# Kernel optimization log

Hardware: AMD Instinct MI355X
Metric: run time of the kernel (lower is better)

Reference implementation:

```python
import jax, jax.numpy as jnp
import numpy as np

N_NODES = 50000
N_EDGES = 200000
IN_C = 128
HID_C = 128
HEADS = 4
OUT_C = 64
NEG_SLOPE = 0.2


def _glorot(key, shape):
    fan_in, fan_out = shape[0], shape[-1]
    limit = np.sqrt(6.0 / (fan_in + fan_out)).astype(np.float32)
    return jax.random.uniform(key, shape, jnp.float32, -limit, limit)


def setup_inputs() -> dict:
    key = jax.random.key(0)
    ks = jax.random.split(key, 32)
    inp = {}
    inp["x"] = jax.random.normal(ks[0], (N_NODES, IN_C), jnp.float32)
    inp["edge_index"] = jax.random.randint(ks[1], (2, N_EDGES), 0, N_NODES, jnp.int64)
    # layer dims: (in_dim, per_head_out, heads)
    dims = [
        (IN_C, HID_C, HEADS),
        (HID_C * HEADS, HID_C, HEADS),
        (HID_C * HEADS, HID_C, HEADS),
        (HID_C * HEADS, OUT_C, 1),
    ]
    concat = [True, True, True, False]
    kidx = 2
    for i, (din, dout, h) in enumerate(dims):
        inp[f"Wl{i}"] = _glorot(ks[kidx], (din, h * dout)); kidx += 1
        inp[f"bl{i}"] = jnp.zeros((h * dout,), jnp.float32)
        inp[f"Wr{i}"] = _glorot(ks[kidx], (din, h * dout)); kidx += 1
        inp[f"br{i}"] = jnp.zeros((h * dout,), jnp.float32)
        inp[f"att{i}"] = _glorot(ks[kidx], (h, dout)); kidx += 1
        inp[f"b{i}"] = jnp.zeros((h * dout if concat[i] else dout,), jnp.float32)
    return inp


def _segment_softmax(e, seg, num_segments):
    # e: [E, H], seg: [E] target-node ids
    m = jax.ops.segment_max(e, seg, num_segments=num_segments)  # [N, H]
    ex = jnp.exp(e - m[seg])
    s = jax.ops.segment_sum(ex, seg, num_segments=num_segments)  # [N, H]
    return ex / (s[seg] + 1e-16)


def _gatv2_layer(x, src, dst, Wl, bl, Wr, br, att, bias, heads, out_c, concat):
    n = x.shape[0]
    xl = (x @ Wl + bl).reshape(n, heads, out_c)  # source transform
    xr = (x @ Wr + br).reshape(n, heads, out_c)  # target transform
    # GATv2 attention: e_ij = a^T LeakyReLU(xl_j + xr_i)
    z = jax.nn.leaky_relu(xl[src] + xr[dst], NEG_SLOPE)  # [E, H, C]
    e = jnp.einsum("ehc,hc->eh", z, att)  # [E, H]
    alpha = _segment_softmax(e, dst, n)  # [E, H]
    out = jax.ops.segment_sum(alpha[:, :, None] * xl[src], dst, num_segments=n)  # [N, H, C]
    out = out.reshape(n, heads * out_c) if concat else out.mean(axis=1)
    return out + bias


def reference(x, edge_index,
              Wl0, bl0, Wr0, br0, att0, b0,
              Wl1, bl1, Wr1, br1, att1, b1,
              Wl2, bl2, Wr2, br2, att2, b2,
              Wl3, bl3, Wr3, br3, att3, b3):
    src, dst = edge_index[0], edge_index[1]
    layers = [
        (Wl0, bl0, Wr0, br0, att0, b0, HEADS, HID_C, True),
        (Wl1, bl1, Wr1, br1, att1, b1, HEADS, HID_C, True),
        (Wl2, bl2, Wr2, br2, att2, b2, HEADS, HID_C, True),
    ]
    h = x
    for (Wl, bl, Wr, br, att, b, nh, dc, cc) in layers:
        h = jax.nn.elu(_gatv2_layer(h, src, dst, Wl, bl, Wr, br, att, b, nh, dc, cc))
    out = _gatv2_layer(h, src, dst, Wl3, bl3, Wr3, br3, att3, b3, 1, OUT_C, False)
    return out
```

## Files before the change

### kernel.cpp

```cpp
#include <hip/hip_runtime.h>
#include <math.h>

#define NNODES 50000
#define NEDGES 200000

typedef unsigned short ushort_t;
using frag8 = __attribute__((ext_vector_type(8))) short;
using facc4 = __attribute__((ext_vector_type(4))) float;

static __device__ __forceinline__ ushort_t f2b(float f) {
  union { float f; unsigned u; } v; v.f = f;
  unsigned r = v.u + 0x7FFFu + ((v.u >> 16) & 1u);
  return (ushort_t)(r >> 16);
}
static __device__ __forceinline__ float b2f(unsigned hi) {
  return __uint_as_float(hi << 16);
}
static __device__ __forceinline__ void unpack8(const int4 v, float* f) {
  f[0] = b2f((unsigned)v.x & 0xFFFFu); f[1] = b2f((unsigned)v.x >> 16);
  f[2] = b2f((unsigned)v.y & 0xFFFFu); f[3] = b2f((unsigned)v.y >> 16);
  f[4] = b2f((unsigned)v.z & 0xFFFFu); f[5] = b2f((unsigned)v.z >> 16);
  f[6] = b2f((unsigned)v.w & 0xFFFFu); f[7] = b2f((unsigned)v.w >> 16);
}
static __device__ __forceinline__ void stf(float* p, float v) { *p = v; }
static __device__ __forceinline__ void stf(ushort_t* p, float v) { *p = f2b(v); }

__global__ void cast_x(const float* __restrict__ x, ushort_t* __restrict__ xb, int total8) {
  int t = blockIdx.x * 256 + threadIdx.x;
  if (t >= total8) return;
  const float4* p = (const float4*)(x + (size_t)t * 8);
  float4 a = p[0], b = p[1];
  int4 w = make_int4(
      (int)((unsigned)f2b(a.x) | ((unsigned)f2b(a.y) << 16)),
      (int)((unsigned)f2b(a.z) | ((unsigned)f2b(a.w) << 16)),
      (int)((unsigned)f2b(b.x) | ((unsigned)f2b(b.y) << 16)),
      (int)((unsigned)f2b(b.z) | ((unsigned)f2b(b.w) << 16)));
  *(int4*)(xb + (size_t)t * 8) = w;
}

__global__ void wt_prep2(const float* __restrict__ Wl, const float* __restrict__ Wr,
                         ushort_t* __restrict__ WtLR, int K, int Mo) {
  int t = blockIdx.x * 256 + threadIdx.x;
  const int tot = K * Mo;
  if (t >= 2 * tot) return;
  const float* W = (t < tot) ? Wl : Wr;
  int u = (t < tot) ? t : t - tot;
  int c = u / K, k = u - c * K;
  WtLR[t] = f2b(W[(size_t)k * Mo + c]);
}

__global__ __launch_bounds__(256) void gemm2_mfma(
    const ushort_t* __restrict__ A, const ushort_t* __restrict__ WtLR,
    const float* __restrict__ bl, const float* __restrict__ br,
    ushort_t* __restrict__ xlb, ushort_t* __restrict__ xrb,
    int N, int K, int Mo, int ncb) {
  __shared__ __align__(16) char smem[34816];
  auto Al = reinterpret_cast<ushort_t(*)[128][8]>(smem);
  auto Bl = reinterpret_cast<ushort_t(*)[128][8]>(smem + 8192);
  auto Cl = reinterpret_cast<ushort_t(*)[136]>(smem);

  const int nwg = gridDim.x;
  const int q = nwg >> 3, r = nwg & 7;
  const int xcd = blockIdx.x & 7, pos = blockIdx.x >> 3;
  const int orig = (xcd < r ? xcd * (q + 1) : r * (q + 1) + (xcd - r) * q) + pos;
  const int rp = orig / ncb, cb = orig - rp * ncb;
  const int brow = rp * 128;
  const int bcol = cb * 128;

  const int tid = threadIdx.x;
  const int wave = tid >> 6, lane = tid & 63;
  const int wr = wave >> 1, wc = wave & 1;
  const int l15 = lane & 15, l4 = lane >> 4;

  facc4 acc[4][4] = {};

  const int srow = tid >> 1;
  const int skb  = (tid & 1) * 2;
  for (int k0 = 0; k0 < K; k0 += 32) {
    {
      const int grow = brow + srow;
      int4 a0, a1;
      if (grow < N) {
        const int4* pa = (const int4*)(A + (size_t)grow * K + k0 + skb * 8);
        a0 = pa[0]; a1 = pa[1];
      } else {
        a0 = a1 = make_int4(0, 0, 0, 0);
      }
      *(int4*)&Al[skb + 0][srow][0] = a0;
      *(int4*)&Al[skb + 1][srow][0] = a1;
      const int4* pb = (const int4*)(WtLR + (size_t)(bcol + srow) * K + k0 + skb * 8);
      int4 b0 = pb[0], b1 = pb[1];
      *(int4*)&Bl[skb + 0][srow][0] = b0;
      *(int4*)&Bl[skb + 1][srow][0] = b1;
    }
    __syncthreads();
    frag8 af[4], bfg[4];
    #pragma unroll
    for (int i = 0; i < 4; ++i)
      af[i] = *(const frag8*)&Al[l4][wr * 64 + i * 16 + l15][0];
    #pragma unroll
    for (int j = 0; j < 4; ++j)
      bfg[j] = *(const frag8*)&Bl[l4][wc * 64 + j * 16 + l15][0];
    #pragma unroll
    for (int i = 0; i < 4; ++i)
      #pragma unroll
      for (int j = 0; j < 4; ++j)
        acc[i][j] = __builtin_amdgcn_mfma_f32_16x16x32_bf16(af[i], bfg[j], acc[i][j], 0, 0, 0);
    __syncthreads();
  }

  #pragma unroll
  for (int j = 0; j < 4; ++j) {
    const int lcol = wc * 64 + j * 16 + l15;
    const int col2 = bcol + lcol;
    const float bv = (col2 < Mo) ? bl[col2] : br[col2 - Mo];
    #pragma unroll
    for (int i = 0; i < 4; ++i) {
      const int lrow = wr * 64 + i * 16 + l4 * 4;
      #pragma unroll
      for (int rr = 0; rr < 4; ++rr)
        Cl[lrow + rr][lcol] = f2b(acc[i][j][rr] + bv);
    }
  }
  __syncthreads();
  {
    const int row = tid >> 1;
    const int half = tid & 1;
    const int grow = brow + row;
    if (grow < N) {
      const int colb = half * 64;
      const int col2 = bcol + colb;
      const bool isL = col2 < Mo;
      ushort_t* dst = (isL ? xlb : xrb) + (size_t)grow * Mo + (isL ? col2 : col2 - Mo);
      #pragma unroll
      for (int k = 0; k < 8; ++k) {
        int4 v = *(const int4*)&Cl[row][colb + k * 8];
        *(int4*)(dst + k * 8) = v;
      }
    }
  }
}

__global__ void csr_zero(int* __restrict__ deg) {
  int t = blockIdx.x * blockDim.x + threadIdx.x;
  if (t < NNODES) deg[t] = 0;
}
__global__ void csr_hist(const int* __restrict__ ei, int* __restrict__ deg) {
  int e = blockIdx.x * blockDim.x + threadIdx.x;
  if (e >= NEDGES) return;
  atomicAdd(&deg[ei[NEDGES + e]], 1);
}

#define SCAN_TPB 256
#define SCAN_EPT 4
#define SCAN_CHUNK (SCAN_TPB * SCAN_EPT)
#define SCAN_BLK ((NNODES + SCAN_CHUNK - 1) / SCAN_CHUNK)

__global__ __launch_bounds__(SCAN_TPB) void scan_k1(const int* __restrict__ deg,
                                                    int* __restrict__ bsum) {
  __shared__ int sd[SCAN_TPB];
  const int tid = threadIdx.x;
  const int tbase = blockIdx.x * SCAN_CHUNK + tid * SCAN_EPT;
  int s = 0;
  #pragma unroll
  for (int j = 0; j < SCAN_EPT; ++j) {
    int idx = tbase + j;
    if (idx < NNODES) s += deg[idx];
  }
  sd[tid] = s;
  __syncthreads();
  for (int d = SCAN_TPB / 2; d > 0; d >>= 1) {
    if (tid < d) sd[tid] += sd[tid + d];
    __syncthreads();
  }
  if (tid == 0) bsum[blockIdx.x] = sd[0];
}

__global__ __launch_bounds__(64) void scan_k2(const int* __restrict__ bsum,
                                              int* __restrict__ bpref,
                                              int* __restrict__ off) {
  __shared__ int sd[64];
  const int tid = threadIdx.x;
  sd[tid] = (tid < SCAN_BLK) ? bsum[tid] : 0;
  __syncthreads();
  for (int d = 1; d < 64; d <<= 1) {
    int t = (tid >= d) ? sd[tid - d] : 0;
    __syncthreads();
    sd[tid] += t;
    __syncthreads();
  }
  if (tid < SCAN_BLK) bpref[tid] = (tid == 0) ? 0 : sd[tid - 1];
  if (tid == 0) off[NNODES] = NEDGES;
}

__global__ __launch_bounds__(SCAN_TPB) void scan_k3(const int* __restrict__ deg,
                                                    const int* __restrict__ bpref,
                                                    int* __restrict__ off,
                                                    int* __restrict__ pos) {
  __shared__ int sd[SCAN_TPB];
  const int tid = threadIdx.x;
  const int tbase = blockIdx.x * SCAN_CHUNK + tid * SCAN_EPT;
  int v[SCAN_EPT];
  int s = 0;
  #pragma unroll
  for (int j = 0; j < SCAN_EPT; ++j) {
    int idx = tbase + j;
    v[j] = (idx < NNODES) ? deg[idx] : 0;
    s += v[j];
  }
  sd[tid] = s;
  __syncthreads();
  for (int d = 1; d < SCAN_TPB; d <<= 1) {
    int t = (tid >= d) ? sd[tid - d] : 0;
    __syncthreads();
    sd[tid] += t;
    __syncthreads();
  }
  int run = bpref[blockIdx.x] + ((tid == 0) ? 0 : sd[tid - 1]);
  #pragma unroll
  for (int j = 0; j < SCAN_EPT; ++j) {
    int idx = tbase + j;
    if (idx < NNODES) { off[idx] = run; pos[idx] = run; run += v[j]; }
  }
}

__global__ void csr_fill(const int* __restrict__ ei, int* __restrict__ pos,
                         int* __restrict__ eids) {
  int e = blockIdx.x * blockDim.x + threadIdx.x;
  if (e >= NEDGES) return;
  int p = atomicAdd(&pos[ei[NEDGES + e]], 1);
  eids[p] = e;
}

template<int H, int C, bool ELU, typename TO>
__global__ __launch_bounds__(256) void csr_fused(
    const int* __restrict__ off, const int* __restrict__ eids,
    const int* __restrict__ ei, const ushort_t* __restrict__ xl,
    const ushort_t* __restrict__ xr, const float* __restrict__ att,
    const float* __restrict__ bias, TO* __restrict__ out) {
  constexpr int HC = H * C;
  constexpr int CPL = HC / 64;
  constexpr int GROUP = C / CPL;
  const int n = (blockIdx.x * blockDim.x + threadIdx.x) >> 6;
  const int lane = threadIdx.x & 63;
  if (n >= NNODES) return;
  const int s0 = off[n], s1 = off[n + 1];

  float xrr[CPL], atr[CPL];
  if constexpr (CPL == 8) {
    unpack8(*(const int4*)(xr + (size_t)n * HC + lane * 8), xrr);
    const float4 a0 = *(const float4*)(att + lane * 8);
    const float4 a1 = *(const float4*)(att + lane * 8 + 4);
    atr[0] = a0.x; atr[1] = a0.y; atr[2] = a0.z; atr[3] = a0.w;
    atr[4] = a1.x; atr[5] = a1.y; atr[6] = a1.z; atr[7] = a1.w;
  } else {
    xrr[0] = b2f(xr[(size_t)n * HC + lane]);
    atr[0] = att[lane];
  }

  float m = -1e30f, s = 0.f;
  float acc[CPL] = {};

  int4 vnext = make_int4(0, 0, 0, 0);
  ushort_t unext = 0;
  if (s0 < s1) {
    const int srcn = ei[eids[s0]];
    if constexpr (CPL == 8) vnext = *(const int4*)(xl + (size_t)srcn * HC + lane * 8);
    else                    unext = xl[(size_t)srcn * HC + lane];
  }
  for (int i = s0; i < s1; ++i) {
    int4 vcur = vnext; ushort_t ucur = unext;
    if (i + 1 < s1) {
      const int srcn = ei[eids[i + 1]];
      if constexpr (CPL == 8) vnext = *(const int4*)(xl + (size_t)srcn * HC + lane * 8);
      else                    unext = xl[(size_t)srcn * HC + lane];
    }
    float zl[CPL];
    if constexpr (CPL == 8) unpack8(vcur, zl);
    else zl[0] = b2f(ucur);
    float e = 0.f;
    #pragma unroll
    for (int c = 0; c < CPL; ++c) {
      float z = zl[c] + xrr[c];
      z = (z > 0.f) ? z : 0.2f * z;
      e += z * atr[c];
    }
    #pragma unroll
    for (int o = 1; o < GROUP; o <<= 1)
      e += __shfl_xor(e, o, 64);
    if (e > m) {
      const float scale = __expf(m - e);
      s *= scale;
      #pragma unroll
      for (int c = 0; c < CPL; ++c) acc[c] *= scale;
      m = e;
    }
    const float w = __expf(e - m);
    s += w;
    #pragma unroll
    for (int c = 0; c < CPL; ++c) acc[c] += w * zl[c];
  }
  const float inv = 1.f / (s + 1e-16f);
  TO* po = out + (size_t)n * HC + lane * CPL;
  #pragma unroll
  for (int c = 0; c < CPL; ++c) {
    float v = acc[c] * inv + bias[lane * CPL + c];
    if (ELU) v = v > 0.f ? v : (__expf(v) - 1.f);
    stf(&po[c], v);
  }
}

__global__ void report_ws(float* __restrict__ out, float v) { out[0] = v; }

extern "C" void kernel_launch(void* const* d_in, const int* in_sizes, int n_in,
                              void* d_out, int out_size, void* d_ws, size_t ws_size,
                              hipStream_t stream) {
  const float* x  = (const float*)d_in[0];
  const int*   ei = (const int*)d_in[1];
  float* out = (float*)d_out;
  char* ws = (char*)d_ws;

  ushort_t* hbuf = (ushort_t*)(ws);
  ushort_t* xlb  = (ushort_t*)(ws + 51200000ull);
  ushort_t* xrb  = (ushort_t*)(ws + 102400000ull);
  ushort_t* xb   = (ushort_t*)(ws + 153600000ull);
  ushort_t* WtLR = (ushort_t*)(ws + 166400000ull);
  int* bsum  = (int*)(ws + 168500000ull);
  int* bpref = (int*)(ws + 168501024ull);
  int* coff  = (int*)(ws + 168600000ull);
  int* cpos  = (int*)(ws + 168800008ull);
  int* cdeg  = (int*)(ws + 169000012ull);
  int* eids  = (int*)(ws + 169200016ull);

  if (ws_size < 170000016ull) {
    report_ws<<<1, 1, 0, stream>>>(out, (float)ws_size);
    return;
  }

  cast_x<<<(NNODES * 128 / 8 + 255) / 256, 256, 0, stream>>>(x, xb, NNODES * 128 / 8);
  csr_zero<<<(NNODES + 255) / 256, 256, 0, stream>>>(cdeg);
  csr_hist<<<(NEDGES + 255) / 256, 256, 0, stream>>>(ei, cdeg);
  scan_k1<<<SCAN_BLK, SCAN_TPB, 0, stream>>>(cdeg, bsum);
  scan_k2<<<1, 64, 0, stream>>>(bsum, bpref, coff);
  scan_k3<<<SCAN_BLK, SCAN_TPB, 0, stream>>>(cdeg, bpref, coff, cpos);
  csr_fill<<<(NEDGES + 255) / 256, 256, 0, stream>>>(ei, cpos, eids);

  const int ngrid = (NNODES * 64 + 255) / 256;
  const int nrp = (NNODES + 127) / 128;

  for (int layer = 0; layer < 4; ++layer) {
    const int base = 2 + layer * 6;
    const float* Wl  = (const float*)d_in[base + 0];
    const float* bl  = (const float*)d_in[base + 1];
    const float* Wr  = (const float*)d_in[base + 2];
    const float* br  = (const float*)d_in[base + 3];
    const float* att = (const float*)d_in[base + 4];
    const float* b   = (const float*)d_in[base + 5];

    const ushort_t* A = (layer == 0) ? xb : hbuf;
    const int K  = (layer == 0) ? 128 : 512;
    const int Mo = (layer == 3) ? 64 : 512;
    const int ncb = 2 * Mo / 128;

    wt_prep2<<<(2 * K * Mo + 255) / 256, 256, 0, stream>>>(Wl, Wr, WtLR, K, Mo);

    gemm2_mfma<<<ncb * nrp, 256, 0, stream>>>(A, WtLR, bl, br, xlb, xrb,
                                              NNODES, K, Mo, ncb);

    if (layer < 3) {
      csr_fused<4, 128, true, ushort_t><<<ngrid, 256, 0, stream>>>(
          coff, eids, ei, xlb, xrb, att, b, hbuf);
    } else {
      csr_fused<1, 64, false, float><<<ngrid, 256, 0, stream>>>(
          coff, eids, ei, xlb, xrb, att, b, out);
    }
  }
}
```

Before: 528.9 us.

## Use direct global-to-LDS loads with K=64 tiles and padded LDS in GEMM

The GEMM now loads A and B tiles with global_load_lds (16-byte direct-to-LDS transfers) instead of staging through registers, and doubles the K step per iteration to 64 so there are half as many barriers. LDS rows are padded (129 and 140 strides) to reduce bank conflicts, and the epilogue writes C in two 64-row halves so the output buffer fits in the smaller shared allocation. Out-of-range rows are clamped rather than zero-filled, and the extra barriers in the epilogue add some synchronisation.

```diff
diff --git a/kernel.cpp b/kernel.cpp
--- a/kernel.cpp
+++ b/kernel.cpp
@@ -7,6 +7,10 @@
 typedef unsigned short ushort_t;
 using frag8 = __attribute__((ext_vector_type(8))) short;
 using facc4 = __attribute__((ext_vector_type(4))) float;
+
+#define GLL16(g, l) __builtin_amdgcn_global_load_lds(                      \
+    (const __attribute__((address_space(1))) void*)(g),                    \
+    (__attribute__((address_space(3))) void*)(l), 16, 0, 0)
 
 static __device__ __forceinline__ ushort_t f2b(float f) {
   union { float f; unsigned u; } v; v.f = f;
@@ -54,10 +58,12 @@
     const float* __restrict__ bl, const float* __restrict__ br,
     ushort_t* __restrict__ xlb, ushort_t* __restrict__ xrb,
     int N, int K, int Mo, int ncb) {
-  __shared__ __align__(16) char smem[34816];
-  auto Al = reinterpret_cast<ushort_t(*)[128][8]>(smem);
-  auto Bl = reinterpret_cast<ushort_t(*)[128][8]>(smem + 8192);
-  auto Cl = reinterpret_cast<ushort_t(*)[136]>(smem);
+  __shared__ __align__(16) char smem[33024];
+  auto Al = reinterpret_cast<ushort_t(*)[129][8]>(smem);
+  auto Bl = reinterpret_cast<ushort_t(*)[129][8]>(smem + 16512);
+  auto Cl = reinterpret_cast<ushort_t(*)[140]>(smem);
+  char* ldsA = (char*)smem;
+  char* ldsB = (char*)smem + 16512;
 
   const int nwg = gridDim.x;
   const int q = nwg >> 3, r = nwg & 7;
@@ -68,76 +74,81 @@
   const int bcol = cb * 128;
 
   const int tid = threadIdx.x;
-  const int wave = tid >> 6, lane = tid & 63;
-  const int wr = wave >> 1, wc = wave & 1;
+  const int w = tid >> 6, lane = tid & 63;
+  const int wr = w >> 1, wc = w & 1;
   const int l15 = lane & 15, l4 = lane >> 4;
 
   facc4 acc[4][4] = {};
 
-  const int srow = tid >> 1;
-  const int skb  = (tid & 1) * 2;
-  for (int k0 = 0; k0 < K; k0 += 32) {
+  int ra0 = brow + lane;        if (ra0 > N - 1) ra0 = N - 1;
+  int ra1 = brow + 64 + lane;   if (ra1 > N - 1) ra1 = N - 1;
+  const ushort_t* pA0 = A + (size_t)ra0 * K;
+  const ushort_t* pA1 = A + (size_t)ra1 * K;
+  const ushort_t* pB0 = WtLR + (size_t)(bcol + lane) * K;
+  const ushort_t* pB1 = WtLR + (size_t)(bcol + 64 + lane) * K;
+
+  for (int k0 = 0; k0 < K; k0 += 64) {
+    #pragma unroll
+    for (int c = 0; c < 4; ++c) {
+      const int kb = 2 * w + (c >> 1);
+      const int rh = c & 1;
+      const int ko = k0 + kb * 8;
+      GLL16((rh ? pA1 : pA0) + ko, ldsA + kb * 2064 + rh * 1024);
+      GLL16((rh ? pB1 : pB0) + ko, ldsB + kb * 2064 + rh * 1024);
+    }
+    __syncthreads();
+    #pragma unroll
+    for (int kk = 0; kk < 2; ++kk) {
+      frag8 af[4], bfg[4];
+      #pragma unroll
+      for (int i = 0; i < 4; ++i)
+        af[i] = *(const frag8*)&Al[kk * 4 + l4][wr * 64 + i * 16 + l15][0];
+      #pragma unroll
+      for (int j = 0; j < 4; ++j)
+        bfg[j] = *(const frag8*)&Bl[kk * 4 + l4][wc * 64 + j * 16 + l15][0];
+      #pragma unroll
+      for (int i = 0; i < 4; ++i)
+        #pragma unroll
+        for (int j = 0; j < 4; ++j)
+          acc[i][j] = __builtin_amdgcn_mfma_f32_16x16x32_bf16(af[i], bfg[j], acc[i][j], 0, 0, 0);
+    }
+    __syncthreads();
+  }
+
+  #pragma unroll
+  for (int half = 0; half < 2; ++half) {
+    if (wr == half) {
+      #pragma unroll
+      for (int j = 0; j < 4; ++j) {
+        const int lcol = wc * 64 + j * 16 + l15;
+        const int col2 = bcol + lcol;
+        const float bv = (col2 < Mo) ? bl[col2] : br[col2 - Mo];
+        #pragma unroll
+        for (int i = 0; i < 4; ++i) {
+          const int lrow = i * 16 + l4 * 4;
+          #pragma unroll
+          for (int rr = 0; rr < 4; ++rr)
+            Cl[lrow + rr][lcol] = f2b(acc[i][j][rr] + bv);
+        }
+      }
+    }
+    __syncthreads();
     {
-      const int grow = brow + srow;
-      int4 a0, a1;
+      const int row = tid >> 2, cq = tid & 3;
+      const int grow = brow + half * 64 + row;
       if (grow < N) {
-        const int4* pa = (const int4*)(A + (size_t)grow * K + k0 + skb * 8);
-        a0 = pa[0]; a1 = pa[1];
-      } else {
-        a0 = a1 = make_int4(0, 0, 0, 0);
+        const int colb = cq * 32;
+        const int col2 = bcol + colb;
+        const bool isL = col2 < Mo;
+        ushort_t* dst = (isL ? xlb : xrb) + (size_t)grow * Mo + (isL ? col2 : col2 - Mo);
+        #pragma unroll
+        for (int k = 0; k < 4; ++k) {
+          int4 v = *(const int4*)&Cl[row][colb + k * 8];
+          *(int4*)(dst + k * 8) = v;
+        }
       }
-      *(int4*)&Al[skb + 0][srow][0] = a0;
-      *(int4*)&Al[skb + 1][srow][0] = a1;
-      const int4* pb = (const int4*)(WtLR + (size_t)(bcol + srow) * K + k0 + skb * 8);
-      int4 b0 = pb[0], b1 = pb[1];
-      *(int4*)&Bl[skb + 0][srow][0] = b0;
-      *(int4*)&Bl[skb + 1][srow][0] = b1;
-    }
-    __syncthreads();
-    frag8 af[4], bfg[4];
-    #pragma unroll
-    for (int i = 0; i < 4; ++i)
-      af[i] = *(const frag8*)&Al[l4][wr * 64 + i * 16 + l15][0];
-    #pragma unroll
-    for (int j = 0; j < 4; ++j)
-      bfg[j] = *(const frag8*)&Bl[l4][wc * 64 + j * 16 + l15][0];
-    #pragma unroll
-    for (int i = 0; i < 4; ++i)
-      #pragma unroll
-      for (int j = 0; j < 4; ++j)
-        acc[i][j] = __builtin_amdgcn_mfma_f32_16x16x32_bf16(af[i], bfg[j], acc[i][j], 0, 0, 0);
-    __syncthreads();
-  }
-
-  #pragma unroll
-  for (int j = 0; j < 4; ++j) {
-    const int lcol = wc * 64 + j * 16 + l15;
-    const int col2 = bcol + lcol;
-    const float bv = (col2 < Mo) ? bl[col2] : br[col2 - Mo];
-    #pragma unroll
-    for (int i = 0; i < 4; ++i) {
-      const int lrow = wr * 64 + i * 16 + l4 * 4;
-      #pragma unroll
-      for (int rr = 0; rr < 4; ++rr)
-        Cl[lrow + rr][lcol] = f2b(acc[i][j][rr] + bv);
-    }
-  }
-  __syncthreads();
-  {
-    const int row = tid >> 1;
-    const int half = tid & 1;
-    const int grow = brow + row;
-    if (grow < N) {
-      const int colb = half * 64;
-      const int col2 = bcol + colb;
-      const bool isL = col2 < Mo;
-      ushort_t* dst = (isL ? xlb : xrb) + (size_t)grow * Mo + (isL ? col2 : col2 - Mo);
-      #pragma unroll
-      for (int k = 0; k < 8; ++k) {
-        int4 v = *(const int4*)&Cl[row][colb + k * 8];
-        *(int4*)(dst + k * 8) = v;
-      }
-    }
+    }
+    __syncthreads();
   }
 }
 
```

After: 630.6 us. +19.2%, slower.

## Add double-buffered direct-to-LDS GEMM for layer 1 and store source ids in CSR

Applied to the files above, without the earlier changes.

Adds a new GEMM kernel that loads A and weight tiles straight into LDS with global_load_lds and double-buffers them, prefetching two K-steps ahead so loads overlap MFMA work. It is used only for layer 1; the other layers keep the original GEMM. Separately, the CSR fill now stores source node ids directly instead of edge ids, which removes one dependent indirect load per edge in the aggregation kernel. The new GEMM uses hand-written waitcnt and barrier sequencing and clamps out-of-range rows, so its correctness depends on that scheduling.

```diff
diff --git a/kernel.cpp b/kernel.cpp
--- a/kernel.cpp
+++ b/kernel.cpp
@@ -7,6 +7,10 @@
 typedef unsigned short ushort_t;
 using frag8 = __attribute__((ext_vector_type(8))) short;
 using facc4 = __attribute__((ext_vector_type(4))) float;
+
+#define GLL16(g, l) __builtin_amdgcn_global_load_lds(                      \
+    (const __attribute__((address_space(1))) void*)(g),                    \
+    (__attribute__((address_space(3))) void*)(l), 16, 0, 0)
 
 static __device__ __forceinline__ ushort_t f2b(float f) {
   union { float f; unsigned u; } v; v.f = f;
@@ -49,7 +53,7 @@
   WtLR[t] = f2b(W[(size_t)k * Mo + c]);
 }
 
-__global__ __launch_bounds__(256) void gemm2_mfma(
+__global__ __launch_bounds__(256) void gemm2_base(
     const ushort_t* __restrict__ A, const ushort_t* __restrict__ WtLR,
     const float* __restrict__ bl, const float* __restrict__ br,
     ushort_t* __restrict__ xlb, ushort_t* __restrict__ xrb,
@@ -68,8 +72,8 @@
   const int bcol = cb * 128;
 
   const int tid = threadIdx.x;
-  const int wave = tid >> 6, lane = tid & 63;
-  const int wr = wave >> 1, wc = wave & 1;
+  const int w = tid >> 6, lane = tid & 63;
+  const int wr = w >> 1, wc = w & 1;
   const int l15 = lane & 15, l4 = lane >> 4;
 
   facc4 acc[4][4] = {};
@@ -141,6 +145,123 @@
   }
 }
 
+__global__ __launch_bounds__(256) void gemm2_pipe(
+    const ushort_t* __restrict__ A, const ushort_t* __restrict__ WtLR,
+    const float* __restrict__ bl, const float* __restrict__ br,
+    ushort_t* __restrict__ xlb, ushort_t* __restrict__ xrb,
+    int N, int K, int Mo, int ncb) {
+  __shared__ __align__(16) char smem[34816];
+  auto Cl = reinterpret_cast<ushort_t(*)[136]>(smem);
+
+  const int nwg = gridDim.x;
+  const int q = nwg >> 3, r = nwg & 7;
+  const int xcd = blockIdx.x & 7, pos = blockIdx.x >> 3;
+  const int orig = (xcd < r ? xcd * (q + 1) : r * (q + 1) + (xcd - r) * q) + pos;
+  const int rp = orig / ncb, cb = orig - rp * ncb;
+  const int brow = rp * 128;
+  const int bcol = cb * 128;
+
+  const int tid = threadIdx.x;
+  const int w = tid >> 6, lane = tid & 63;
+  const int wr = w >> 1, wc = w & 1;
+  const int l15 = lane & 15, l4 = lane >> 4;
+
+  const ushort_t* gsrc[4];
+  int ldst[4];
+  #pragma unroll
+  for (int c4 = 0; c4 < 4; ++c4) {
+    const int c = w * 4 + c4;
+    if (c < 8) {
+      const int kb = c >> 1, half = c & 1;
+      int rrow = brow + half * 64 + lane;
+      if (rrow > N - 1) rrow = N - 1;
+      gsrc[c4] = A + (size_t)rrow * K + kb * 8;
+      ldst[c4] = c * 1024;
+    } else {
+      const int cB = c - 8;
+      const int kb = cB >> 1, half = cB & 1;
+      const int col = bcol + half * 64 + lane;
+      gsrc[c4] = WtLR + (size_t)col * K + kb * 8;
+      ldst[c4] = 8192 + cB * 1024;
+    }
+  }
+
+  facc4 acc[4][4] = {};
+  const int nt = K >> 5;
+
+  #pragma unroll
+  for (int c4 = 0; c4 < 4; ++c4) GLL16(gsrc[c4], smem + ldst[c4]);
+  #pragma unroll
+  for (int c4 = 0; c4 < 4; ++c4) GLL16(gsrc[c4] + 32, smem + 16384 + ldst[c4]);
+
+  for (int t = 0; t < nt; ++t) {
+    if (t + 1 < nt) asm volatile("s_waitcnt vmcnt(4)" ::: "memory");
+    else            asm volatile("s_waitcnt vmcnt(0)" ::: "memory");
+    __builtin_amdgcn_sched_barrier(0);
+    __builtin_amdgcn_s_barrier();
+    __builtin_amdgcn_sched_barrier(0);
+
+    const int bufb = (t & 1) << 14;
+    const char* Ab = smem + bufb;
+    const char* Bb = smem + bufb + 8192;
+    frag8 af[4], bfg[4];
+    #pragma unroll
+    for (int i = 0; i < 4; ++i)
+      af[i] = *(const frag8*)(Ab + l4 * 2048 + (wr * 64 + i * 16 + l15) * 16);
+    #pragma unroll
+    for (int j = 0; j < 4; ++j)
+      bfg[j] = *(const frag8*)(Bb + l4 * 2048 + (wc * 64 + j * 16 + l15) * 16);
+
+    asm volatile("s_waitcnt lgkmcnt(0)" ::: "memory");
+    __builtin_amdgcn_sched_barrier(0);
+    __builtin_amdgcn_s_barrier();
+    __builtin_amdgcn_sched_barrier(0);
+
+    if (t + 2 < nt) {
+      #pragma unroll
+      for (int c4 = 0; c4 < 4; ++c4)
+        GLL16(gsrc[c4] + (t + 2) * 32, smem + bufb + ldst[c4]);
+    }
+    #pragma unroll
+    for (int i = 0; i < 4; ++i)
+      #pragma unroll
+      for (int j = 0; j < 4; ++j)
+        acc[i][j] = __builtin_amdgcn_mfma_f32_16x16x32_bf16(af[i], bfg[j], acc[i][j], 0, 0, 0);
+  }
+
+  __syncthreads();
+  #pragma unroll
+  for (int j = 0; j < 4; ++j) {
+    const int lcol = wc * 64 + j * 16 + l15;
+    const int col2 = bcol + lcol;
+    const float bv = (col2 < Mo) ? bl[col2] : br[col2 - Mo];
+    #pragma unroll
+    for (int i = 0; i < 4; ++i) {
+      const int lrow = wr * 64 + i * 16 + l4 * 4;
+      #pragma unroll
+      for (int rr = 0; rr < 4; ++rr)
+        Cl[lrow + rr][lcol] = f2b(acc[i][j][rr] + bv);
+    }
+  }
+  __syncthreads();
+  {
+    const int row = tid >> 1;
+    const int half = tid & 1;
+    const int grow = brow + row;
+    if (grow < N) {
+      const int colb = half * 64;
+      const int col2 = bcol + colb;
+      const bool isL = col2 < Mo;
+      ushort_t* dst = (isL ? xlb : xrb) + (size_t)grow * Mo + (isL ? col2 : col2 - Mo);
+      #pragma unroll
+      for (int k = 0; k < 8; ++k) {
+        int4 v = *(const int4*)&Cl[row][colb + k * 8];
+        *(int4*)(dst + k * 8) = v;
+      }
+    }
+  }
+}
+
 __global__ void csr_zero(int* __restrict__ deg) {
   int t = blockIdx.x * blockDim.x + threadIdx.x;
   if (t < NNODES) deg[t] = 0;
@@ -225,19 +346,19 @@
 }
 
 __global__ void csr_fill(const int* __restrict__ ei, int* __restrict__ pos,
-                         int* __restrict__ eids) {
+                         int* __restrict__ srcs) {
   int e = blockIdx.x * blockDim.x + threadIdx.x;
   if (e >= NEDGES) return;
   int p = atomicAdd(&pos[ei[NEDGES + e]], 1);
-  eids[p] = e;
+  srcs[p] = ei[e];
 }
 
 template<int H, int C, bool ELU, typename TO>
 __global__ __launch_bounds__(256) void csr_fused(
-    const int* __restrict__ off, const int* __restrict__ eids,
-    const int* __restrict__ ei, const ushort_t* __restrict__ xl,
-    const ushort_t* __restrict__ xr, const float* __restrict__ att,
-    const float* __restrict__ bias, TO* __restrict__ out) {
+    const int* __restrict__ off, const int* __restrict__ srcs,
+    const ushort_t* __restrict__ xl, const ushort_t* __restrict__ xr,
+    const float* __restrict__ att, const float* __restrict__ bias,
+    TO* __restrict__ out) {
   constexpr int HC = H * C;
   constexpr int CPL = HC / 64;
   constexpr int GROUP = C / CPL;
@@ -264,14 +385,14 @@
   int4 vnext = make_int4(0, 0, 0, 0);
   ushort_t unext = 0;
   if (s0 < s1) {
-    const int srcn = ei[eids[s0]];
+    const int srcn = srcs[s0];
     if constexpr (CPL == 8) vnext = *(const int4*)(xl + (size_t)srcn * HC + lane * 8);
     else                    unext = xl[(size_t)srcn * HC + lane];
   }
   for (int i = s0; i < s1; ++i) {
     int4 vcur = vnext; ushort_t ucur = unext;
     if (i + 1 < s1) {
-      const int srcn = ei[eids[i + 1]];
+      const int srcn = srcs[i + 1];
       if constexpr (CPL == 8) vnext = *(const int4*)(xl + (size_t)srcn * HC + lane * 8);
       else                    unext = xl[(size_t)srcn * HC + lane];
     }
@@ -330,7 +451,7 @@
   int* coff  = (int*)(ws + 168600000ull);
   int* cpos  = (int*)(ws + 168800008ull);
   int* cdeg  = (int*)(ws + 169000012ull);
-  int* eids  = (int*)(ws + 169200016ull);
+  int* srcs  = (int*)(ws + 169200016ull);
 
   if (ws_size < 170000016ull) {
     report_ws<<<1, 1, 0, stream>>>(out, (float)ws_size);
@@ -343,7 +464,7 @@
   scan_k1<<<SCAN_BLK, SCAN_TPB, 0, stream>>>(cdeg, bsum);
   scan_k2<<<1, 64, 0, stream>>>(bsum, bpref, coff);
   scan_k3<<<SCAN_BLK, SCAN_TPB, 0, stream>>>(cdeg, bpref, coff, cpos);
-  csr_fill<<<(NEDGES + 255) / 256, 256, 0, stream>>>(ei, cpos, eids);
+  csr_fill<<<(NEDGES + 255) / 256, 256, 0, stream>>>(ei, cpos, srcs);
 
   const int ngrid = (NNODES * 64 + 255) / 256;
   const int nrp = (NNODES + 127) / 128;
@@ -364,15 +485,20 @@
 
     wt_prep2<<<(2 * K * Mo + 255) / 256, 256, 0, stream>>>(Wl, Wr, WtLR, K, Mo);
 
-    gemm2_mfma<<<ncb * nrp, 256, 0, stream>>>(A, WtLR, bl, br, xlb, xrb,
-                                              NNODES, K, Mo, ncb);
+    if (layer == 1) {
+      gemm2_pipe<<<ncb * nrp, 256, 0, stream>>>(A, WtLR, bl, br, xlb, xrb,
+                                                NNODES, K, Mo, ncb);
+    } else {
+      gemm2_base<<<ncb * nrp, 256, 0, stream>>>(A, WtLR, bl, br, xlb, xrb,
+                                                NNODES, K, Mo, ncb);
+    }
 
     if (layer < 3) {
       csr_fused<4, 128, true, ushort_t><<<ngrid, 256, 0, stream>>>(
-          coff, eids, ei, xlb, xrb, att, b, hbuf);
+          coff, srcs, xlb, xrb, att, b, hbuf);
     } else {
       csr_fused<1, 64, false, float><<<ngrid, 256, 0, stream>>>(
-          coff, eids, ei, xlb, xrb, att, b, out);
-    }
-  }
-}
+          coff, srcs, xlb, xrb, att, b, out);
+    }
+  }
+}
```

New measurement: 531.2 us. About the same (+0.4%).

## Prefetch GEMM tiles two steps ahead and store source ids directly in CSR

Applied to the files above, without the earlier changes.

The GEMM main loop now keeps two register sets of A/B tiles and loads the tile two k-steps ahead while the current tile is staged to LDS and consumed by MFMA. This hides global load latency behind compute, at the cost of more registers. Separately, the CSR fill writes source node ids instead of edge ids. That removes one dependent indirection (ei[eids[i]]) per edge in the aggregation kernel.

```diff
diff --git a/kernel.cpp b/kernel.cpp
--- a/kernel.cpp
+++ b/kernel.cpp
@@ -49,7 +49,7 @@
   WtLR[t] = f2b(W[(size_t)k * Mo + c]);
 }
 
-__global__ __launch_bounds__(256) void gemm2_mfma(
+__global__ __launch_bounds__(256) void gemm2_pf2(
     const ushort_t* __restrict__ A, const ushort_t* __restrict__ WtLR,
     const float* __restrict__ bl, const float* __restrict__ br,
     ushort_t* __restrict__ xlb, ushort_t* __restrict__ xrb,
@@ -68,46 +68,63 @@
   const int bcol = cb * 128;
 
   const int tid = threadIdx.x;
-  const int wave = tid >> 6, lane = tid & 63;
-  const int wr = wave >> 1, wc = wave & 1;
+  const int w = tid >> 6, lane = tid & 63;
+  const int wr = w >> 1, wc = w & 1;
   const int l15 = lane & 15, l4 = lane >> 4;
 
   facc4 acc[4][4] = {};
 
   const int srow = tid >> 1;
   const int skb  = (tid & 1) * 2;
-  for (int k0 = 0; k0 < K; k0 += 32) {
-    {
-      const int grow = brow + srow;
-      int4 a0, a1;
-      if (grow < N) {
-        const int4* pa = (const int4*)(A + (size_t)grow * K + k0 + skb * 8);
-        a0 = pa[0]; a1 = pa[1];
-      } else {
-        a0 = a1 = make_int4(0, 0, 0, 0);
-      }
-      *(int4*)&Al[skb + 0][srow][0] = a0;
-      *(int4*)&Al[skb + 1][srow][0] = a1;
-      const int4* pb = (const int4*)(WtLR + (size_t)(bcol + srow) * K + k0 + skb * 8);
-      int4 b0 = pb[0], b1 = pb[1];
-      *(int4*)&Bl[skb + 0][srow][0] = b0;
-      *(int4*)&Bl[skb + 1][srow][0] = b1;
-    }
-    __syncthreads();
-    frag8 af[4], bfg[4];
-    #pragma unroll
-    for (int i = 0; i < 4; ++i)
-      af[i] = *(const frag8*)&Al[l4][wr * 64 + i * 16 + l15][0];
-    #pragma unroll
-    for (int j = 0; j < 4; ++j)
-      bfg[j] = *(const frag8*)&Bl[l4][wc * 64 + j * 16 + l15][0];
-    #pragma unroll
-    for (int i = 0; i < 4; ++i)
-      #pragma unroll
-      for (int j = 0; j < 4; ++j)
-        acc[i][j] = __builtin_amdgcn_mfma_f32_16x16x32_bf16(af[i], bfg[j], acc[i][j], 0, 0, 0);
-    __syncthreads();
-  }
+  const int grow = brow + srow;
+  const bool rowok = grow < N;
+  const ushort_t* pa = A + (size_t)(rowok ? grow : 0) * K + skb * 8;
+  const ushort_t* pb = WtLR + (size_t)(bcol + srow) * K + skb * 8;
+
+  const int nt = K >> 5;
+
+  int4 a00, a01, b00, b01;
+  int4 a10, a11, b10, b11;
+  if (rowok) { const int4* p = (const int4*)pa; a00 = p[0]; a01 = p[1]; }
+  else       { a00 = a01 = make_int4(0, 0, 0, 0); }
+  { const int4* p = (const int4*)pb; b00 = p[0]; b01 = p[1]; }
+  if (rowok) { const int4* p = (const int4*)(pa + 32); a10 = p[0]; a11 = p[1]; }
+  else       { a10 = a11 = make_int4(0, 0, 0, 0); }
+  { const int4* p = (const int4*)(pb + 32); b10 = p[0]; b11 = p[1]; }
+
+#define PF2_BODY(AS0, AS1, BS0, BS1, T)                                        \
+  {                                                                            \
+    *(int4*)&Al[skb + 0][srow][0] = AS0;                                       \
+    *(int4*)&Al[skb + 1][srow][0] = AS1;                                       \
+    *(int4*)&Bl[skb + 0][srow][0] = BS0;                                       \
+    *(int4*)&Bl[skb + 1][srow][0] = BS1;                                       \
+    if ((T) + 2 < nt) {                                                        \
+      const int k0 = ((T) + 2) * 32;                                           \
+      if (rowok) { const int4* p = (const int4*)(pa + k0); AS0 = p[0]; AS1 = p[1]; } \
+      { const int4* p = (const int4*)(pb + k0); BS0 = p[0]; BS1 = p[1]; }      \
+    }                                                                          \
+    __syncthreads();                                                           \
+    frag8 af[4], bfg[4];                                                       \
+    _Pragma("unroll")                                                          \
+    for (int i = 0; i < 4; ++i)                                                \
+      af[i] = *(const frag8*)&Al[l4][wr * 64 + i * 16 + l15][0];               \
+    _Pragma("unroll")                                                          \
+    for (int j = 0; j < 4; ++j)                                                \
+      bfg[j] = *(const frag8*)&Bl[l4][wc * 64 + j * 16 + l15][0];              \
+    _Pragma("unroll")                                                          \
+    for (int i = 0; i < 4; ++i)                                                \
+      _Pragma("unroll")                                                        \
+      for (int j = 0; j < 4; ++j)                                              \
+        acc[i][j] = __builtin_amdgcn_mfma_f32_16x16x32_bf16(af[i], bfg[j],     \
+                                                            acc[i][j], 0, 0, 0); \
+    __syncthreads();                                                           \
+  }
+
+  for (int t = 0; t < nt; t += 2) {
+    PF2_BODY(a00, a01, b00, b01, t);
+    PF2_BODY(a10, a11, b10, b11, t + 1);
+  }
+#undef PF2_BODY
 
   #pragma unroll
   for (int j = 0; j < 4; ++j) {
@@ -126,12 +143,12 @@
   {
     const int row = tid >> 1;
     const int half = tid & 1;
-    const int grow = brow + row;
-    if (grow < N) {
+    const int growo = brow + row;
+    if (growo < N) {
       const int colb = half * 64;
       const int col2 = bcol + colb;
       const bool isL = col2 < Mo;
-      ushort_t* dst = (isL ? xlb : xrb) + (size_t)grow * Mo + (isL ? col2 : col2 - Mo);
+      ushort_t* dst = (isL ? xlb : xrb) + (size_t)growo * Mo + (isL ? col2 : col2 - Mo);
       #pragma unroll
       for (int k = 0; k < 8; ++k) {
         int4 v = *(const int4*)&Cl[row][colb + k * 8];
@@ -225,19 +242,19 @@
 }
 
 __global__ void csr_fill(const int* __restrict__ ei, int* __restrict__ pos,
-                         int* __restrict__ eids) {
+                         int* __restrict__ srcs) {
   int e = blockIdx.x * blockDim.x + threadIdx.x;
   if (e >= NEDGES) return;
   int p = atomicAdd(&pos[ei[NEDGES + e]], 1);
-  eids[p] = e;
+  srcs[p] = ei[e];
 }
 
 template<int H, int C, bool ELU, typename TO>
 __global__ __launch_bounds__(256) void csr_fused(
-    const int* __restrict__ off, const int* __restrict__ eids,
-    const int* __restrict__ ei, const ushort_t* __restrict__ xl,
-    const ushort_t* __restrict__ xr, const float* __restrict__ att,
-    const float* __restrict__ bias, TO* __restrict__ out) {
+    const int* __restrict__ off, const int* __restrict__ srcs,
+    const ushort_t* __restrict__ xl, const ushort_t* __restrict__ xr,
+    const float* __restrict__ att, const float* __restrict__ bias,
+    TO* __restrict__ out) {
   constexpr int HC = H * C;
   constexpr int CPL = HC / 64;
   constexpr int GROUP = C / CPL;
@@ -264,14 +281,14 @@
   int4 vnext = make_int4(0, 0, 0, 0);
   ushort_t unext = 0;
   if (s0 < s1) {
-    const int srcn = ei[eids[s0]];
+    const int srcn = srcs[s0];
     if constexpr (CPL == 8) vnext = *(const int4*)(xl + (size_t)srcn * HC + lane * 8);
     else                    unext = xl[(size_t)srcn * HC + lane];
   }
   for (int i = s0; i < s1; ++i) {
     int4 vcur = vnext; ushort_t ucur = unext;
     if (i + 1 < s1) {
-      const int srcn = ei[eids[i + 1]];
+      const int srcn = srcs[i + 1];
       if constexpr (CPL == 8) vnext = *(const int4*)(xl + (size_t)srcn * HC + lane * 8);
       else                    unext = xl[(size_t)srcn * HC + lane];
     }
@@ -330,7 +347,7 @@
   int* coff  = (int*)(ws + 168600000ull);
   int* cpos  = (int*)(ws + 168800008ull);
   int* cdeg  = (int*)(ws + 169000012ull);
-  int* eids  = (int*)(ws + 169200016ull);
+  int* srcs  = (int*)(ws + 169200016ull);
 
   if (ws_size < 170000016ull) {
     report_ws<<<1, 1, 0, stream>>>(out, (float)ws_size);
@@ -343,7 +360,7 @@
   scan_k1<<<SCAN_BLK, SCAN_TPB, 0, stream>>>(cdeg, bsum);
   scan_k2<<<1, 64, 0, stream>>>(bsum, bpref, coff);
   scan_k3<<<SCAN_BLK, SCAN_TPB, 0, stream>>>(cdeg, bpref, coff, cpos);
-  csr_fill<<<(NEDGES + 255) / 256, 256, 0, stream>>>(ei, cpos, eids);
+  csr_fill<<<(NEDGES + 255) / 256, 256, 0, stream>>>(ei, cpos, srcs);
 
   const int ngrid = (NNODES * 64 + 255) / 256;
   const int nrp = (NNODES + 127) / 128;
@@ -364,15 +381,15 @@
 
     wt_prep2<<<(2 * K * Mo + 255) / 256, 256, 0, stream>>>(Wl, Wr, WtLR, K, Mo);
 
-    gemm2_mfma<<<ncb * nrp, 256, 0, stream>>>(A, WtLR, bl, br, xlb, xrb,
-                                              NNODES, K, Mo, ncb);
+    gemm2_pf2<<<ncb * nrp, 256, 0, stream>>>(A, WtLR, bl, br, xlb, xrb,
+                                             NNODES, K, Mo, ncb);
 
     if (layer < 3) {
       csr_fused<4, 128, true, ushort_t><<<ngrid, 256, 0, stream>>>(
-          coff, eids, ei, xlb, xrb, att, b, hbuf);
+          coff, srcs, xlb, xrb, att, b, hbuf);
     } else {
       csr_fused<1, 64, false, float><<<ngrid, 256, 0, stream>>>(
-          coff, eids, ei, xlb, xrb, att, b, out);
-    }
-  }
-}
+          coff, srcs, xlb, xrb, att, b, out);
+    }
+  }
+}
```

After: 475.2 us. -10.2%, faster.
